# Optimization experiments

Hardware: AMD Instinct MI355X
Metric: run time of the kernel (lower is better)

Reference implementation:

```python
import jax, jax.numpy as jnp
import numpy as np

# BTT factorization dims: d_in = m1*m2 = 4096, d_out = n1*n2 = 4096, rs = (1, R, 1)
B = 4096
M1 = 64
M2 = 64
N1 = 64
N2 = 64
R = 4  # tt_rank


def setup_inputs() -> dict:
    key = jax.random.key(0)
    kx, k1, k2 = jax.random.split(key, 3)
    # xavier_normal_(W, gain=1/sqrt(fan_in_factor)); fan_in/out of xavier use last two dims
    std1 = (1.0 / (M1 * 1) ** 0.5) * (2.0 / (M1 * 1 + N1 * R)) ** 0.5
    std2 = (1.0 / (M2 * R) ** 0.5) * (2.0 / (M2 * R + N2 * 1)) ** 0.5
    x = jax.random.normal(kx, (B, M1 * M2), dtype=jnp.float32)
    W1 = jax.random.normal(k1, (M2, M1 * 1, N1 * R), dtype=jnp.float32) * std1
    W2 = jax.random.normal(k2, (N1, M2 * R, N2 * 1), dtype=jnp.float32) * std2
    return {"x": x, "W1": W1, "W2": W2}


def reference(x, W1, W2):
    b = x.shape[0]
    # stage 1: contract m1, batched over m2 -> intermediate (b, m2, n1, r2)
    xr = x.reshape(b, M2, M1)                             # (b, m2, m1)
    t = jnp.einsum('bma,mac->bmc', xr, W1)                # (b, m2, n1*r2)
    t = t.reshape(b, M2, N1, R)                           # (b, m2, n1, r2)
    # stage 2: contract (m2, r2), batched over n1 -> (b, n1, n2)
    t = t.transpose(0, 2, 1, 3).reshape(b, N1, M2 * R)    # (b, n1, m2*r2)
    y = jnp.einsum('bnd,ndo->bno', t, W2)                 # (b, n1, n2)
    return y.reshape(b, N1 * N2)
```

## Files before the change

### kernel.cpp

```cpp
#include <hip/hip_runtime.h>

typedef unsigned short u16;
typedef unsigned int u32;
typedef __attribute__((ext_vector_type(8))) short short8;
typedef __attribute__((ext_vector_type(4))) float f32x4;

__device__ __forceinline__ u16 f2bf(float f) {
    union { float f; u32 u; } c; c.f = f;
    u32 u = c.u;
    return (u16)((u + 0x7fffu + ((u >> 16) & 1u)) >> 16);
}

#define MFMA16(A, B, C) __builtin_amdgcn_mfma_f32_16x16x32_bf16((A), (B), (C), 0, 0, 0)

__global__ __launch_bounds__(256) void prep_w(const float* __restrict__ W1,
                                              const float* __restrict__ W2,
                                              u16* __restrict__ W1F,
                                              u16* __restrict__ W2F) {
    __shared__ u16 sh[16384];
    const int bid = blockIdx.x;
    const int t = threadIdx.x;

    if (bid < 64) {
        const int m2 = bid;
        const float4* src = (const float4*)(W1 + (size_t)m2 * 16384);
        #pragma unroll
        for (int s = 0; s < 16; ++s) {
            float4 f = src[s * 256 + t];
            float fv[4] = {f.x, f.y, f.z, f.w};
            #pragma unroll
            for (int e = 0; e < 4; ++e) {
                int elem = (s * 256 + t) * 4 + e;
                int m1 = elem >> 8, c = elem & 255;
                int nb = c >> 5, ct = (c >> 4) & 1, lr = c & 15;
                int ks = m1 >> 5, q = (m1 >> 3) & 3, j = m1 & 7;
                sh[(((((nb * 2 + ct) * 2 + ks) * 4 + q)) << 7) + lr * 8 + j] =
                    f2bf(fv[e]);
            }
        }
        __syncthreads();
        u16* dst = W1F + (size_t)m2 * 16384 + t * 64;
        #pragma unroll
        for (int s = 0; s < 8; ++s)
            *(short8*)(dst + s * 8) = *(const short8*)(&sh[t * 64 + s * 8]);
    } else {
        const int n1 = bid - 64;
        const float4* src = (const float4*)(W2 + (size_t)n1 * 16384);
        #pragma unroll
        for (int s = 0; s < 16; ++s) {
            float4 f = src[s * 256 + t];
            float fv[4] = {f.x, f.y, f.z, f.w};
            #pragma unroll
            for (int e = 0; e < 4; ++e) {
                int elem = (s * 256 + t) * 4 + e;
                int k = elem >> 6, n2 = elem & 63;
                int m2b = k >> 5, q = (k >> 3) & 3, j = k & 7;
                int nt = n2 >> 4, lr = n2 & 15;
                sh[((((m2b * 4 + nt) * 4 + q)) << 7) + lr * 8 + j] = f2bf(fv[e]);
            }
        }
        __syncthreads();
        u16* dst = W2F + (size_t)n1 * 16384 + t * 64;
        #pragma unroll
        for (int s = 0; s < 8; ++s)
            *(short8*)(dst + s * 8) = *(const short8*)(&sh[t * 64 + s * 8]);
    }
}

__global__ __launch_bounds__(512) void btt_f64(const float* __restrict__ x,
                                               const u16* __restrict__ W1F,
                                               const u16* __restrict__ W2F,
                                               float* __restrict__ out) {
    __shared__ u16 t_lds[2][64 * 260];

    const int tid = threadIdx.x;
    const int w = tid >> 6;
    const int lane = tid & 63;
    const int q = lane >> 4;
    const int lr = lane & 15;
    const int bt = blockIdx.x & 63;
    const int nb = blockIdx.x >> 6;
    const int n1 = nb * 8 + w;

    const f32x4 fz = {0.f, 0.f, 0.f, 0.f};
    f32x4 acc2[4][4];
    #pragma unroll
    for (int i = 0; i < 4; ++i)
        #pragma unroll
        for (int j = 0; j < 4; ++j) acc2[i][j] = fz;

    for (int m2b = 0; m2b < 8; ++m2b) {
        const int m2 = m2b * 8 + w;
        const int p = m2b & 1;

        short8 a1[2][2];
        {
            const u16* pw = W1F + ((size_t)m2 * 8 + nb) * 2048 + lane * 8;
            #pragma unroll
            for (int ct = 0; ct < 2; ++ct)
                #pragma unroll
                for (int ks = 0; ks < 2; ++ks)
                    a1[ct][ks] = *(const short8*)(pw + (ct * 2 + ks) * 512);
        }
        short8 b2[4];
        {
            const u16* pw = W2F + (size_t)n1 * 16384 + m2b * 2048 + lane * 8;
            #pragma unroll
            for (int nt = 0; nt < 4; ++nt)
                b2[nt] = *(const short8*)(pw + nt * 512);
        }

        short8 ax[4][2];
        #pragma unroll
        for (int bl = 0; bl < 4; ++bl)
            #pragma unroll
            for (int ks = 0; ks < 2; ++ks) {
                const float* px = x + (size_t)(bt * 64 + bl * 16 + lr) * 4096 +
                                  m2 * 64 + ks * 32 + q * 8;
                float4 ua = *(const float4*)(px);
                float4 ub = *(const float4*)(px + 4);
                short8 r;
                r[0] = (short)f2bf(ua.x); r[1] = (short)f2bf(ua.y);
                r[2] = (short)f2bf(ua.z); r[3] = (short)f2bf(ua.w);
                r[4] = (short)f2bf(ub.x); r[5] = (short)f2bf(ub.y);
                r[6] = (short)f2bf(ub.z); r[7] = (short)f2bf(ub.w);
                ax[bl][ks] = r;
            }

        f32x4 acc1[2][4];
        #pragma unroll
        for (int ct = 0; ct < 2; ++ct)
            #pragma unroll
            for (int bl = 0; bl < 4; ++bl) acc1[ct][bl] = fz;
        #pragma unroll
        for (int ks = 0; ks < 2; ++ks)
            #pragma unroll
            for (int ct = 0; ct < 2; ++ct)
                #pragma unroll
                for (int bl = 0; bl < 4; ++bl)
                    acc1[ct][bl] = MFMA16(a1[ct][ks], ax[bl][ks], acc1[ct][bl]);

        #pragma unroll
        for (int ct = 0; ct < 2; ++ct)
            #pragma unroll
            for (int bl = 0; bl < 4; ++bl) {
                int off = (bl * 16 + lr) * 260 + w * 32 + ct * 16 + q * 4;
                u32 lo = (u32)f2bf(acc1[ct][bl][0]) | ((u32)f2bf(acc1[ct][bl][1]) << 16);
                u32 hi = (u32)f2bf(acc1[ct][bl][2]) | ((u32)f2bf(acc1[ct][bl][3]) << 16);
                *(uint2*)(&t_lds[p][off]) = make_uint2(lo, hi);
            }

        __syncthreads();

        short8 a2[4];
        #pragma unroll
        for (int bl = 0; bl < 4; ++bl) {
            int base = (bl * 16 + lr) * 260 + (2 * q) * 32 + w * 4;
            union { short8 v; uint2 u[2]; } tmp;
            tmp.u[0] = *(const uint2*)(&t_lds[p][base]);
            tmp.u[1] = *(const uint2*)(&t_lds[p][base + 32]);
            a2[bl] = tmp.v;
        }
        #pragma unroll
        for (int bl = 0; bl < 4; ++bl)
            #pragma unroll
            for (int nt = 0; nt < 4; ++nt)
                acc2[bl][nt] = MFMA16(a2[bl], b2[nt], acc2[bl][nt]);
    }

    #pragma unroll
    for (int bl = 0; bl < 4; ++bl)
        #pragma unroll
        for (int nt = 0; nt < 4; ++nt)
            #pragma unroll
            for (int g = 0; g < 4; ++g) {
                long row = bt * 64 + bl * 16 + q * 4 + g;
                long col = (long)n1 * 64 + nt * 16 + lr;
                out[row * 4096 + col] = acc2[bl][nt][g];
            }
}

__global__ __launch_bounds__(512) void btt_nows(const float* __restrict__ x,
                                                const float* __restrict__ W1,
                                                const float* __restrict__ W2,
                                                float* __restrict__ out) {
    __shared__ u16 t_lds[64 * 260];
    const int tid = threadIdx.x;
    const int w = tid >> 6;
    const int lane = tid & 63;
    const int q = lane >> 4;
    const int lr = lane & 15;
    const int bt = blockIdx.x & 63;
    const int nb = blockIdx.x >> 6;
    const int n1 = nb * 8 + w;

    const f32x4 fz = {0.f, 0.f, 0.f, 0.f};
    f32x4 acc2[4][4];
    #pragma unroll
    for (int i = 0; i < 4; ++i)
        #pragma unroll
        for (int j = 0; j < 4; ++j) acc2[i][j] = fz;

    for (int m2b = 0; m2b < 8; ++m2b) {
        const int m2 = m2b * 8 + w;
        short8 ax[4][2];
        #pragma unroll
        for (int bl = 0; bl < 4; ++bl)
            #pragma unroll
            for (int ks = 0; ks < 2; ++ks) {
                const float* p = x + (size_t)(bt * 64 + bl * 16 + lr) * 4096 +
                                 m2 * 64 + ks * 32 + q * 8;
                float4 ua = *(const float4*)(p);
                float4 ub = *(const float4*)(p + 4);
                short8 r;
                r[0] = (short)f2bf(ua.x); r[1] = (short)f2bf(ua.y);
                r[2] = (short)f2bf(ua.z); r[3] = (short)f2bf(ua.w);
                r[4] = (short)f2bf(ub.x); r[5] = (short)f2bf(ub.y);
                r[6] = (short)f2bf(ub.z); r[7] = (short)f2bf(ub.w);
                ax[bl][ks] = r;
            }
        short8 bw1[2][2];
        #pragma unroll
        for (int ct = 0; ct < 2; ++ct)
            #pragma unroll
            for (int ks = 0; ks < 2; ++ks)
                #pragma unroll
                for (int j = 0; j < 8; ++j)
                    bw1[ct][ks][j] = (short)f2bf(W1[m2 * 16384 +
                                                    (ks * 32 + q * 8 + j) * 256 +
                                                    nb * 32 + ct * 16 + lr]);
        f32x4 acc1[4][2];
        #pragma unroll
        for (int bl = 0; bl < 4; ++bl)
            #pragma unroll
            for (int ct = 0; ct < 2; ++ct) acc1[bl][ct] = fz;
        #pragma unroll
        for (int ks = 0; ks < 2; ++ks)
            #pragma unroll
            for (int bl = 0; bl < 4; ++bl)
                #pragma unroll
                for (int ct = 0; ct < 2; ++ct)
                    acc1[bl][ct] = MFMA16(ax[bl][ks], bw1[ct][ks], acc1[bl][ct]);

        __syncthreads();
        #pragma unroll
        for (int bl = 0; bl < 4; ++bl)
            #pragma unroll
            for (int ct = 0; ct < 2; ++ct)
                #pragma unroll
                for (int g = 0; g < 4; ++g)
                    t_lds[(bl * 16 + q * 4 + g) * 260 + w * 32 + ct * 16 + lr] =
                        f2bf(acc1[bl][ct][g]);
        __syncthreads();

        short8 a2[4];
        #pragma unroll
        for (int bl = 0; bl < 4; ++bl) {
            int base = (bl * 16 + lr) * 260 + (2 * q) * 32 + w * 4;
            union { short8 v; uint2 u[2]; } tmp;
            tmp.u[0] = *(const uint2*)(&t_lds[base]);
            tmp.u[1] = *(const uint2*)(&t_lds[base + 32]);
            a2[bl] = tmp.v;
        }
        short8 b2[4];
        #pragma unroll
        for (int nt = 0; nt < 4; ++nt)
            #pragma unroll
            for (int j = 0; j < 8; ++j)
                b2[nt][j] = (short)f2bf(W2[n1 * 16384 +
                                           (m2b * 32 + q * 8 + j) * 64 +
                                           nt * 16 + lr]);
        #pragma unroll
        for (int bl = 0; bl < 4; ++bl)
            #pragma unroll
            for (int nt = 0; nt < 4; ++nt)
                acc2[bl][nt] = MFMA16(a2[bl], b2[nt], acc2[bl][nt]);
    }

    #pragma unroll
    for (int bl = 0; bl < 4; ++bl)
        #pragma unroll
        for (int nt = 0; nt < 4; ++nt)
            #pragma unroll
            for (int g = 0; g < 4; ++g) {
                long row = bt * 64 + bl * 16 + q * 4 + g;
                long col = (long)n1 * 64 + nt * 16 + lr;
                out[row * 4096 + col] = acc2[bl][nt][g];
            }
}

extern "C" void kernel_launch(void* const* d_in, const int* in_sizes, int n_in,
                              void* d_out, int out_size, void* d_ws, size_t ws_size,
                              hipStream_t stream) {
    const float* x  = (const float*)d_in[0];
    const float* W1 = (const float*)d_in[1];
    const float* W2 = (const float*)d_in[2];
    float* out = (float*)d_out;

    const size_t N_W1F = (size_t)64 * 16384;
    const size_t N_W2F = (size_t)64 * 16384;
    const size_t WS_NEED = (N_W1F + N_W2F) * sizeof(u16);

    if (ws_size >= WS_NEED) {
        u16* W1F = (u16*)d_ws;
        u16* W2F = W1F + N_W1F;
        prep_w<<<128, 256, 0, stream>>>(W1, W2, W1F, W2F);
        btt_f64<<<512, 512, 0, stream>>>(x, W1F, W2F, out);
    } else {
        btt_nows<<<512, 512, 0, stream>>>(x, W1, W2, out);
    }
}
```

Measured before the change: 199.2 us.

## Pre-convert x to bf16 fragment layout and prefetch next x tile in main kernel

Adds a prep pass that converts x from fp32 to bf16 and writes it in MFMA fragment order into workspace. The main kernel then loads ready-made bf16 fragments and prefetches the next m2 block's x fragments into registers, which overlaps those loads with the current stage-1 compute. It also moves the W2 loads after the barrier and replaces __syncthreads with an explicit lgkmcnt wait plus s_barrier. The cost is an extra full pass over x (a 64MB read and a 32MB write) and higher register pressure; the main kernel now reads 32MB of bf16 x instead of 64MB of fp32.

```diff
diff --git a/kernel.cpp b/kernel.cpp
--- a/kernel.cpp
+++ b/kernel.cpp
@@ -13,16 +13,40 @@
 
 #define MFMA16(A, B, C) __builtin_amdgcn_mfma_f32_16x16x32_bf16((A), (B), (C), 0, 0, 0)
 
-__global__ __launch_bounds__(256) void prep_w(const float* __restrict__ W1,
-                                              const float* __restrict__ W2,
-                                              u16* __restrict__ W1F,
-                                              u16* __restrict__ W2F) {
+__global__ __launch_bounds__(256) void prep(const float* __restrict__ x,
+                                            const float* __restrict__ W1,
+                                            const float* __restrict__ W2,
+                                            u16* __restrict__ XF,
+                                            u16* __restrict__ W1F,
+                                            u16* __restrict__ W2F) {
     __shared__ u16 sh[16384];
     const int bid = blockIdx.x;
     const int t = threadIdx.x;
 
-    if (bid < 64) {
-        const int m2 = bid;
+    if (bid < 512) {
+        const int bt = bid >> 3, m2g = bid & 7;
+        const int w = t >> 6, l = t & 63;
+        const int m2i = l >> 3;
+        const int ks = (l >> 2) & 1;
+        const int q = l & 3;
+        const float* base = x + ((size_t)bt * 64) * 4096 + m2g * 512 + l * 8;
+        u16* tilebase = XF + ((size_t)(bt * 64 + m2g * 8 + m2i)) * 4096;
+        #pragma unroll
+        for (int rr = 0; rr < 16; ++rr) {
+            const int row = rr * 4 + w;
+            const float* p = base + (size_t)row * 4096;
+            float4 f0 = *(const float4*)(p);
+            float4 f1 = *(const float4*)(p + 4);
+            short8 r;
+            r[0] = (short)f2bf(f0.x); r[1] = (short)f2bf(f0.y);
+            r[2] = (short)f2bf(f0.z); r[3] = (short)f2bf(f0.w);
+            r[4] = (short)f2bf(f1.x); r[5] = (short)f2bf(f1.y);
+            r[6] = (short)f2bf(f1.z); r[7] = (short)f2bf(f1.w);
+            const int bl = row >> 4, lr = row & 15;
+            *(short8*)(tilebase + (((bl * 2 + ks) * 4 + q) << 7) + lr * 8) = r;
+        }
+    } else if (bid < 576) {
+        const int m2 = bid - 512;
         const float4* src = (const float4*)(W1 + (size_t)m2 * 16384);
         #pragma unroll
         for (int s = 0; s < 16; ++s) {
@@ -44,7 +68,7 @@
         for (int s = 0; s < 8; ++s)
             *(short8*)(dst + s * 8) = *(const short8*)(&sh[t * 64 + s * 8]);
     } else {
-        const int n1 = bid - 64;
+        const int n1 = bid - 576;
         const float4* src = (const float4*)(W2 + (size_t)n1 * 16384);
         #pragma unroll
         for (int s = 0; s < 16; ++s) {
@@ -67,10 +91,10 @@
     }
 }
 
-__global__ __launch_bounds__(512) void btt_f64(const float* __restrict__ x,
-                                               const u16* __restrict__ W1F,
-                                               const u16* __restrict__ W2F,
-                                               float* __restrict__ out) {
+__global__ __launch_bounds__(512, 4) void btt_p(const u16* __restrict__ XF,
+                                                const u16* __restrict__ W1F,
+                                                const u16* __restrict__ W2F,
+                                                float* __restrict__ out) {
     __shared__ u16 t_lds[2][64 * 260];
 
     const int tid = threadIdx.x;
@@ -89,6 +113,15 @@
         #pragma unroll
         for (int j = 0; j < 4; ++j) acc2[i][j] = fz;
 
+    const u16* xbase = XF + ((size_t)bt * 64 + w) * 4096 + lane * 8;
+
+    short8 b1c[4][2];
+    #pragma unroll
+    for (int bl = 0; bl < 4; ++bl)
+        #pragma unroll
+        for (int ks = 0; ks < 2; ++ks)
+            b1c[bl][ks] = *(const short8*)(xbase + (bl * 2 + ks) * 512);
+
     for (int m2b = 0; m2b < 8; ++m2b) {
         const int m2 = m2b * 8 + w;
         const int p = m2b & 1;
@@ -102,30 +135,15 @@
                 for (int ks = 0; ks < 2; ++ks)
                     a1[ct][ks] = *(const short8*)(pw + (ct * 2 + ks) * 512);
         }
-        short8 b2[4];
+        short8 b1n[4][2];
         {
-            const u16* pw = W2F + (size_t)n1 * 16384 + m2b * 2048 + lane * 8;
-            #pragma unroll
-            for (int nt = 0; nt < 4; ++nt)
-                b2[nt] = *(const short8*)(pw + nt * 512);
-        }
-
-        short8 ax[4][2];
-        #pragma unroll
-        for (int bl = 0; bl < 4; ++bl)
-            #pragma unroll
-            for (int ks = 0; ks < 2; ++ks) {
-                const float* px = x + (size_t)(bt * 64 + bl * 16 + lr) * 4096 +
-                                  m2 * 64 + ks * 32 + q * 8;
-                float4 ua = *(const float4*)(px);
-                float4 ub = *(const float4*)(px + 4);
-                short8 r;
-                r[0] = (short)f2bf(ua.x); r[1] = (short)f2bf(ua.y);
-                r[2] = (short)f2bf(ua.z); r[3] = (short)f2bf(ua.w);
-                r[4] = (short)f2bf(ub.x); r[5] = (short)f2bf(ub.y);
-                r[6] = (short)f2bf(ub.z); r[7] = (short)f2bf(ub.w);
-                ax[bl][ks] = r;
-            }
+            const u16* xn = xbase + (size_t)(((m2b + 1) & 7) * 8) * 4096;
+            #pragma unroll
+            for (int bl = 0; bl < 4; ++bl)
+                #pragma unroll
+                for (int ks = 0; ks < 2; ++ks)
+                    b1n[bl][ks] = *(const short8*)(xn + (bl * 2 + ks) * 512);
+        }
 
         f32x4 acc1[2][4];
         #pragma unroll
@@ -138,7 +156,7 @@
             for (int ct = 0; ct < 2; ++ct)
                 #pragma unroll
                 for (int bl = 0; bl < 4; ++bl)
-                    acc1[ct][bl] = MFMA16(a1[ct][ks], ax[bl][ks], acc1[ct][bl]);
+                    acc1[ct][bl] = MFMA16(a1[ct][ks], b1c[bl][ks], acc1[ct][bl]);
 
         #pragma unroll
         for (int ct = 0; ct < 2; ++ct)
@@ -150,7 +168,11 @@
                 *(uint2*)(&t_lds[p][off]) = make_uint2(lo, hi);
             }
 
-        __syncthreads();
+        __builtin_amdgcn_sched_barrier(0);
+        asm volatile("s_waitcnt lgkmcnt(0)" ::: "memory");
+        __builtin_amdgcn_sched_barrier(0);
+        __builtin_amdgcn_s_barrier();
+        __builtin_amdgcn_sched_barrier(0);
 
         short8 a2[4];
         #pragma unroll
@@ -161,11 +183,24 @@
             tmp.u[1] = *(const uint2*)(&t_lds[p][base + 32]);
             a2[bl] = tmp.v;
         }
+        short8 b2[4];
+        {
+            const u16* pw = W2F + (size_t)n1 * 16384 + m2b * 2048 + lane * 8;
+            #pragma unroll
+            for (int nt = 0; nt < 4; ++nt)
+                b2[nt] = *(const short8*)(pw + nt * 512);
+        }
         #pragma unroll
         for (int bl = 0; bl < 4; ++bl)
             #pragma unroll
             for (int nt = 0; nt < 4; ++nt)
                 acc2[bl][nt] = MFMA16(a2[bl], b2[nt], acc2[bl][nt]);
+
+        #pragma unroll
+        for (int bl = 0; bl < 4; ++bl)
+            #pragma unroll
+            for (int ks = 0; ks < 2; ++ks)
+                b1c[bl][ks] = b1n[bl][ks];
     }
 
     #pragma unroll
@@ -299,13 +334,15 @@
 
     const size_t N_W1F = (size_t)64 * 16384;
     const size_t N_W2F = (size_t)64 * 16384;
-    const size_t WS_NEED = (N_W1F + N_W2F) * sizeof(u16);
+    const size_t N_XF  = (size_t)4096 * 4096;
+    const size_t WS_NEED = (N_W1F + N_W2F + N_XF) * sizeof(u16);
 
     if (ws_size >= WS_NEED) {
         u16* W1F = (u16*)d_ws;
         u16* W2F = W1F + N_W1F;
-        prep_w<<<128, 256, 0, stream>>>(W1, W2, W1F, W2F);
-        btt_f64<<<512, 512, 0, stream>>>(x, W1F, W2F, out);
+        u16* XF  = W2F + N_W2F;
+        prep<<<512 + 64 + 64, 256, 0, stream>>>(x, W1, W2, XF, W1F, W2F);
+        btt_p<<<512, 512, 0, stream>>>(XF, W1F, W2F, out);
     } else {
         btt_nows<<<512, 512, 0, stream>>>(x, W1, W2, out);
     }
```

Measured after the change: 241.7 us. 1.21x slower.

## Coalesce x loads and transpose through per-wave swizzled LDS scratch

Applied to the files above, without the earlier changes.

x is now read with each 16-lane group fetching one contiguous 256-byte row chunk, instead of strided per-lane 32-byte reads. The data is converted to bf16 and staged through a per-wave XOR-swizzled LDS scratch to rebuild the MFMA operand layout. The double-buffered t_lds becomes a single buffer guarded by an extra __syncthreads per iteration. This aims to cut global-memory transaction overhead on x, at the cost of extra LDS traffic, explicit waitcnts, and one more block barrier per step.

```diff
diff --git a/kernel.cpp b/kernel.cpp
--- a/kernel.cpp
+++ b/kernel.cpp
@@ -9,6 +9,10 @@
     union { float f; u32 u; } c; c.f = f;
     u32 u = c.u;
     return (u16)((u + 0x7fffu + ((u >> 16) & 1u)) >> 16);
+}
+
+__device__ __forceinline__ u32 pack2(float a, float b) {
+    return (u32)f2bf(a) | ((u32)f2bf(b) << 16);
 }
 
 #define MFMA16(A, B, C) __builtin_amdgcn_mfma_f32_16x16x32_bf16((A), (B), (C), 0, 0, 0)
@@ -67,20 +71,28 @@
     }
 }
 
-__global__ __launch_bounds__(512) void btt_f64(const float* __restrict__ x,
-                                               const u16* __restrict__ W1F,
-                                               const u16* __restrict__ W2F,
-                                               float* __restrict__ out) {
-    __shared__ u16 t_lds[2][64 * 260];
+__global__ __launch_bounds__(512) void btt_x(const float* __restrict__ x,
+                                             const u16* __restrict__ W1F,
+                                             const u16* __restrict__ W2F,
+                                             float* __restrict__ out) {
+    __shared__ u16 t_lds[64 * 260];
+    __shared__ u16 xscr[8][2080];
 
     const int tid = threadIdx.x;
     const int w = tid >> 6;
     const int lane = tid & 63;
     const int q = lane >> 4;
     const int lr = lane & 15;
+    const int lo = lane & 15;
     const int bt = blockIdx.x & 63;
     const int nb = blockIdx.x >> 6;
     const int n1 = nb * 8 + w;
+
+    const int wks = lo >> 3;
+    const int wq  = (lo >> 1) & 3;
+    const int wj0 = (lo & 1) * 4;
+    const int wswz = (wks * 4 + wq) & 7;
+    u16* scr = xscr[w];
 
     const f32x4 fz = {0.f, 0.f, 0.f, 0.f};
     f32x4 acc2[4][4];
@@ -91,7 +103,12 @@
 
     for (int m2b = 0; m2b < 8; ++m2b) {
         const int m2 = m2b * 8 + w;
-        const int p = m2b & 1;
+        const float* xt = x + ((size_t)bt * 64 + q) * 4096 + m2 * 64 + lo * 4;
+
+        float4 f0[8];
+        #pragma unroll
+        for (int i8 = 0; i8 < 8; ++i8)
+            f0[i8] = *(const float4*)(xt + (size_t)(i8 * 4) * 4096);
 
         short8 a1[2][2];
         {
@@ -110,21 +127,52 @@
                 b2[nt] = *(const short8*)(pw + nt * 512);
         }
 
-        short8 ax[4][2];
-        #pragma unroll
-        for (int bl = 0; bl < 4; ++bl)
+        #pragma unroll
+        for (int i8 = 0; i8 < 8; ++i8) {
+            int rl = i8 * 4 + q;
+            int bl_l = (rl >> 4) & 1;
+            int lrw = rl & 15;
+            int off = ((bl_l * 2 + wks) * 4 + wq) * 128 + ((lrw ^ wswz) * 8) + wj0;
+            uint2 d = make_uint2(pack2(f0[i8].x, f0[i8].y),
+                                 pack2(f0[i8].z, f0[i8].w));
+            *(uint2*)(&scr[off]) = d;
+        }
+
+        float4 f1[8];
+        #pragma unroll
+        for (int i8 = 0; i8 < 8; ++i8)
+            f1[i8] = *(const float4*)(xt + (size_t)(32 + i8 * 4) * 4096);
+
+        asm volatile("s_waitcnt lgkmcnt(0)" ::: "memory");
+        short8 b1[4][2];
+        #pragma unroll
+        for (int bl = 0; bl < 2; ++bl)
             #pragma unroll
             for (int ks = 0; ks < 2; ++ks) {
-                const float* px = x + (size_t)(bt * 64 + bl * 16 + lr) * 4096 +
-                                  m2 * 64 + ks * 32 + q * 8;
-                float4 ua = *(const float4*)(px);
-                float4 ub = *(const float4*)(px + 4);
-                short8 r;
-                r[0] = (short)f2bf(ua.x); r[1] = (short)f2bf(ua.y);
-                r[2] = (short)f2bf(ua.z); r[3] = (short)f2bf(ua.w);
-                r[4] = (short)f2bf(ub.x); r[5] = (short)f2bf(ub.y);
-                r[6] = (short)f2bf(ub.z); r[7] = (short)f2bf(ub.w);
-                ax[bl][ks] = r;
+                int off = ((bl * 2 + ks) * 4 + q) * 128 +
+                          ((lr ^ ((ks * 4 + q) & 7)) * 8);
+                b1[bl][ks] = *(const short8*)(&scr[off]);
+            }
+        asm volatile("s_waitcnt lgkmcnt(0)" ::: "memory");
+
+        #pragma unroll
+        for (int i8 = 0; i8 < 8; ++i8) {
+            int rl = 32 + i8 * 4 + q;
+            int bl_l = (rl >> 4) & 1;
+            int lrw = rl & 15;
+            int off = ((bl_l * 2 + wks) * 4 + wq) * 128 + ((lrw ^ wswz) * 8) + wj0;
+            uint2 d = make_uint2(pack2(f1[i8].x, f1[i8].y),
+                                 pack2(f1[i8].z, f1[i8].w));
+            *(uint2*)(&scr[off]) = d;
+        }
+        asm volatile("s_waitcnt lgkmcnt(0)" ::: "memory");
+        #pragma unroll
+        for (int bl = 2; bl < 4; ++bl)
+            #pragma unroll
+            for (int ks = 0; ks < 2; ++ks) {
+                int off = (((bl & 1) * 2 + ks) * 4 + q) * 128 +
+                          ((lr ^ ((ks * 4 + q) & 7)) * 8);
+                b1[bl][ks] = *(const short8*)(&scr[off]);
             }
 
         f32x4 acc1[2][4];
@@ -138,16 +186,18 @@
             for (int ct = 0; ct < 2; ++ct)
                 #pragma unroll
                 for (int bl = 0; bl < 4; ++bl)
-                    acc1[ct][bl] = MFMA16(a1[ct][ks], ax[bl][ks], acc1[ct][bl]);
+                    acc1[ct][bl] = MFMA16(a1[ct][ks], b1[bl][ks], acc1[ct][bl]);
+
+        __syncthreads();
 
         #pragma unroll
         for (int ct = 0; ct < 2; ++ct)
             #pragma unroll
             for (int bl = 0; bl < 4; ++bl) {
                 int off = (bl * 16 + lr) * 260 + w * 32 + ct * 16 + q * 4;
-                u32 lo = (u32)f2bf(acc1[ct][bl][0]) | ((u32)f2bf(acc1[ct][bl][1]) << 16);
-                u32 hi = (u32)f2bf(acc1[ct][bl][2]) | ((u32)f2bf(acc1[ct][bl][3]) << 16);
-                *(uint2*)(&t_lds[p][off]) = make_uint2(lo, hi);
+                u32 lov = pack2(acc1[ct][bl][0], acc1[ct][bl][1]);
+                u32 hiv = pack2(acc1[ct][bl][2], acc1[ct][bl][3]);
+                *(uint2*)(&t_lds[off]) = make_uint2(lov, hiv);
             }
 
         __syncthreads();
@@ -157,8 +207,8 @@
         for (int bl = 0; bl < 4; ++bl) {
             int base = (bl * 16 + lr) * 260 + (2 * q) * 32 + w * 4;
             union { short8 v; uint2 u[2]; } tmp;
-            tmp.u[0] = *(const uint2*)(&t_lds[p][base]);
-            tmp.u[1] = *(const uint2*)(&t_lds[p][base + 32]);
+            tmp.u[0] = *(const uint2*)(&t_lds[base]);
+            tmp.u[1] = *(const uint2*)(&t_lds[base + 32]);
             a2[bl] = tmp.v;
         }
         #pragma unroll
@@ -305,7 +355,7 @@
         u16* W1F = (u16*)d_ws;
         u16* W2F = W1F + N_W1F;
         prep_w<<<128, 256, 0, stream>>>(W1, W2, W1F, W2F);
-        btt_f64<<<512, 512, 0, stream>>>(x, W1F, W2F, out);
+        btt_x<<<512, 512, 0, stream>>>(x, W1F, W2F, out);
     } else {
         btt_nows<<<512, 512, 0, stream>>>(x, W1, W2, out);
     }
```

After: 190.3 us. 1.05x faster.
